# Kernel optimization log

Measured on AMD Instinct MI355X. Metric: run time of the kernel, lower is better.

## Reference

```python
import jax, jax.numpy as jnp
import numpy as np

OBS = 128; N_AGENT = 16; N_ACTION = 8; N_LAYER = 2; HID = 128
GE = 256; LE = 256; F1 = 512; F2 = 512


def _edges(batch_size, n):
    # all ordered pairs (i, j), i != j, within each sample; GCNConv adds self-loops
    i, j = np.meshgrid(np.arange(n), np.arange(n), indexing='ij')
    m = i != j
    src0, dst0 = i[m], j[m]                      # [n*(n-1)]
    off = (np.arange(batch_size) * n)[:, None]
    src = (src0[None, :] + off).reshape(-1)
    dst = (dst0[None, :] + off).reshape(-1)
    return jnp.asarray(src, jnp.int32), jnp.asarray(dst, jnp.int32)


def setup_inputs() -> dict:
    key = jax.random.key(0)
    ks = jax.random.split(key, 16)
    g = lambda k, shp, fan: jax.random.normal(k, shp, jnp.float32) / np.sqrt(fan)
    return {
        'obs_j': jax.random.normal(ks[0], (2048, N_AGENT, OBS), jnp.float32),
        'W_pre': g(ks[1], (OBS, HID), OBS), 'b_pre': jnp.zeros((HID,), jnp.float32),
        'W_gcn': g(ks[2], (N_LAYER, HID, HID), HID), 'b_gcn': jnp.zeros((N_LAYER, HID), jnp.float32),
        'W_post': g(ks[3], (HID, GE), HID), 'b_post': jnp.zeros((GE,), jnp.float32),
        'W_loc': g(ks[4], (OBS, LE), OBS), 'b_loc': jnp.zeros((LE,), jnp.float32),
        'W1': g(ks[5], (GE + LE, F1), GE + LE), 'b1': jnp.zeros((F1,), jnp.float32),
        'W2': g(ks[6], (F1, F2), F1), 'b2': jnp.zeros((F2,), jnp.float32),
        'W3': g(ks[7], (F2, N_ACTION), F2), 'b3': jnp.zeros((N_ACTION,), jnp.float32),
    }


def reference(obs_j, W_pre, b_pre, W_gcn, b_gcn, W_post, b_post,
              W_loc, b_loc, W1, b1, W2, b2, W3, b3):
    B, n, _ = obs_j.shape
    N = B * n
    obs = obs_j.reshape(N, OBS)
    x = jax.nn.relu(obs @ W_pre + b_pre)          # [N, HID]

    src, dst = _edges(B, n)
    # GCNConv with self-loops on a fully-connected graph: deg = n for every node,
    # edge norm = 1/sqrt(deg_i*deg_j) = 1/n for every (A+I) edge.
    inv_n = jnp.float32(1.0) / n
    for l in range(N_LAYER):
        h = x @ W_gcn[l]                          # lin (no bias inside propagate)
        agg = jax.ops.segment_sum(h[src], dst, num_segments=N)  # neighbor gather/scatter
        x = jax.nn.relu((agg + h) * inv_n + b_gcn[l])            # + self-loop msg, bias

    g = x.reshape(B, n, HID).mean(axis=1)         # global_mean_pool over each graph
    g = jax.nn.relu(g @ W_post + b_post)          # [B, GE]
    loc = jax.nn.relu(obs @ W_loc + b_loc)        # [B*n, LE]
    gi = jnp.repeat(g, n, axis=0)                 # repeat_interleave over agents
    z = jnp.concatenate([gi, loc], axis=1)
    z = jax.nn.relu(z @ W1 + b1)
    z = jax.nn.relu(z @ W2 + b2)
    q = z @ W3 + b3
    return q.reshape(B, n, N_ACTION)
```

## Files before the change

kernel.cpp:

```cpp
#include <hip/hip_runtime.h>
#include <hip/hip_bf16.h>
#include <stdint.h>

typedef __bf16 bf16;
typedef __bf16 bf16x4 __attribute__((ext_vector_type(4)));
typedef __bf16 bf16x8 __attribute__((ext_vector_type(8)));
typedef float f32x4 __attribute__((ext_vector_type(4)));

#define MFMA(a, b, c) __builtin_amdgcn_mfma_f32_16x16x32_bf16(a, b, c, 0, 0, 0)
#define GL(p) ((const __attribute__((address_space(1))) void*)(p))
#define SH(p) ((__attribute__((address_space(3))) void*)(p))

__device__ inline void tp(const float* W, bf16* WT, int id, int shiftK, int N) {
  int K = 1 << shiftK;
  int n = id >> shiftK;
  int k = id & (K - 1);
  WT[id] = (bf16)W[(size_t)k * N + n];
}

__global__ __launch_bounds__(256) void prep_all(
    const float* __restrict__ W1, const float* __restrict__ W2,
    bf16* __restrict__ W1T, bf16* __restrict__ W2T,
    const float* __restrict__ Wpre, const float* __restrict__ Wloc,
    const float* __restrict__ Wgcn, const float* __restrict__ Wpost,
    bf16* __restrict__ WpreLocT, bf16* __restrict__ Wg0T, bf16* __restrict__ Wg1T,
    bf16* __restrict__ WpostT,
    const float* __restrict__ bpre, const float* __restrict__ bloc,
    float* __restrict__ biasPL, float* __restrict__ outq) {
  __shared__ bf16 tile[64 * 68];
  int blk = blockIdx.x;
  int tid = threadIdx.x;
  if (blk < 128) {
    const float* W = (blk < 64) ? W1 : W2;
    bf16* WT = (blk < 64) ? W1T : W2T;
    int t = blk & 63;
    int tk0 = (t >> 3) * 64, tn0 = (t & 7) * 64;
#pragma unroll
    for (int p = 0; p < 4; p++) {
      int kr = p * 16 + (tid >> 4), nc = (tid & 15) * 4;
      float4 f = *(const float4*)(W + (size_t)(tk0 + kr) * 512 + tn0 + nc);
      bf16x4 v; v[0] = (bf16)f.x; v[1] = (bf16)f.y; v[2] = (bf16)f.z; v[3] = (bf16)f.w;
      *(bf16x4*)&tile[kr * 68 + nc] = v;
    }
    __syncthreads();
#pragma unroll
    for (int p = 0; p < 4; p++) {
      int nr = p * 16 + (tid >> 4), kc = (tid & 15) * 4;
      bf16x4 v;
#pragma unroll
      for (int i = 0; i < 4; i++) v[i] = tile[(kc + i) * 68 + nr];
      *(bf16x4*)(WT + (size_t)(tn0 + nr) * 512 + tk0 + kc) = v;
    }
    return;
  }
  blk -= 128;
  if (blk < 448) {
    int id = blk * 256 + tid;
    if (id < 16384) { tp(Wpre, WpreLocT, id, 7, 128); return; } id -= 16384;
    if (id < 32768) { tp(Wloc, WpreLocT + 16384, id, 7, 256); return; } id -= 32768;
    if (id < 16384) { tp(Wgcn, Wg0T, id, 7, 128); return; } id -= 16384;
    if (id < 16384) { tp(Wgcn + 16384, Wg1T, id, 7, 128); return; } id -= 16384;
    tp(Wpost, WpostT, id, 7, 256);
    return;
  }
  blk -= 448;
  if (blk == 0) {
    if (tid < 128) biasPL[tid] = bpre[tid];
    biasPL[128 + tid] = bloc[tid];
    return;
  }
  blk -= 1;
  float4 z = {0.f, 0.f, 0.f, 0.f};
#pragma unroll
  for (int i = 0; i < 4; i++)
    ((float4*)outq)[(size_t)blk * 1024 + i * 256 + tid] = z;
}

__global__ __launch_bounds__(256, 4) void k1c(
    const float* __restrict__ obs, const bf16* __restrict__ WpreLocT,
    const float* __restrict__ biasPL,
    const bf16* __restrict__ Wg0T, const bf16* __restrict__ Wg1T,
    const bf16* __restrict__ WpostT, const float* __restrict__ b_gcn,
    const float* __restrict__ b_post,
    const bf16* __restrict__ W1T, const float* __restrict__ b1,
    bf16* __restrict__ loc, float* __restrict__ h) {
  __shared__ bf16 smem[16384];

  const int tid = threadIdx.x;
  const int id = blockIdx.x;
  const int s = id >> 3;
  const int n_idx = s % 3;
  const int m0 = ((id & 7) + 8 * (s / 3)) * 128;
  const int n0 = n_idx * 128;

  f32x4 acc[4][4] = {};
  const int lane = tid & 63, wave = tid >> 6;
  const int wm = (wave >> 1) * 64, wn = (wave & 1) * 64;
  const int lm = lane & 15, quad = lane >> 4;

  float4 pa[4];

  auto loadA = [&](int kt) {
#pragma unroll
    for (int it = 0; it < 2; it++) {
      int idx = it * 256 + tid;
      int row = idx >> 2;
      int c = idx & 3;
      int cv = c ^ ((row >> 1) & 3);
      const float* src = obs + (size_t)(m0 + row) * 128 + kt * 32 + cv * 8;
      pa[it * 2] = *(const float4*)src;
      pa[it * 2 + 1] = *(const float4*)(src + 4);
    }
  };
  auto stageB = [&](int kt, int buf) {
    bf16* Bd = smem + buf * 8192 + 4096;
#pragma unroll
    for (int it = 0; it < 2; it++) {
      int idx = it * 256 + tid;
      int row = idx >> 2;
      int c = idx & 3;
      int cv = c ^ ((row >> 1) & 3);
      const bf16* gb = WpreLocT + (size_t)(n0 + row) * 128 + kt * 32 + cv * 8;
      __builtin_amdgcn_global_load_lds(GL(gb), SH(&Bd[(idx & ~63) * 8]), 16, 0, 0);
    }
  };
  auto commitA = [&](int buf) {
    bf16* Ad = smem + buf * 8192;
#pragma unroll
    for (int it = 0; it < 2; it++) {
      int idx = it * 256 + tid;
      int row = idx >> 2;
      int c = idx & 3;
      float4 f0 = pa[it * 2], f1 = pa[it * 2 + 1];
      bf16x8 v;
      v[0] = (bf16)f0.x; v[1] = (bf16)f0.y; v[2] = (bf16)f0.z; v[3] = (bf16)f0.w;
      v[4] = (bf16)f1.x; v[5] = (bf16)f1.y; v[6] = (bf16)f1.z; v[7] = (bf16)f1.w;
      *(bf16x8*)&Ad[row * 32 + c * 8] = v;
    }
  };
  auto compute = [&](int buf) {
    const bf16* Ar = smem + buf * 8192;
    const bf16* Br = smem + buf * 8192 + 4096;
    bf16x8 a[4], b[4];
#pragma unroll
    for (int i = 0; i < 4; i++) {
      int r = wm + lm + i * 16;
      a[i] = *(const bf16x8*)&Ar[r * 32 + ((quad ^ ((r >> 1) & 3)) * 8)];
    }
#pragma unroll
    for (int j = 0; j < 4; j++) {
      int r = wn + lm + j * 16;
      b[j] = *(const bf16x8*)&Br[r * 32 + ((quad ^ ((r >> 1) & 3)) * 8)];
    }
#pragma unroll
    for (int i = 0; i < 4; i++)
#pragma unroll
      for (int j = 0; j < 4; j++)
        acc[i][j] = MFMA(a[i], b[j], acc[i][j]);
  };

  loadA(0); stageB(0, 0); commitA(0);
  __syncthreads();
#pragma unroll
  for (int i = 0; i < 4; ++i) {
    if (i + 1 < 4) { loadA(i + 1); stageB(i + 1, (i + 1) & 1); }
    compute(i & 1);
    if (i + 1 < 4) commitA((i + 1) & 1);
    __syncthreads();
  }

  if (n_idx == 0) {
    bf16* xs = smem;
    bf16* x2 = smem + 2176;
    bf16* gS = smem + 4352;
#pragma unroll
    for (int i = 0; i < 4; i++) {
      int sl = (wave >> 1) * 4 + i;
#pragma unroll
      for (int j = 0; j < 4; j++) {
        int col = wn + j * 16 + lm;
        float bb = biasPL[col];
        float v = 0.f;
#pragma unroll
        for (int r = 0; r < 4; r++) v += fmaxf(acc[i][j][r] + bb, 0.f);
        v += __shfl_xor(v, 16);
        v += __shfl_xor(v, 32);
        if (quad == 0) xs[sl * 136 + col] = (bf16)(v * 0.0625f);
        else if (quad == 1) xs[(8 + sl) * 136 + col] = (bf16)0.f;
      }
    }
    __syncthreads();
    {
      f32x4 c2[2] = {};
#pragma unroll
      for (int ku = 0; ku < 4; ++ku) {
        bf16x8 a = *(const bf16x8*)&xs[lm * 136 + (ku * 4 + quad) * 8];
#pragma unroll
        for (int jn = 0; jn < 2; ++jn) {
          int col = (wave * 2 + jn) * 16 + lm;
          bf16x8 b = *(const bf16x8*)&Wg0T[(size_t)col * 128 + ku * 32 + quad * 8];
          c2[jn] = MFMA(a, b, c2[jn]);
        }
      }
      __syncthreads();
#pragma unroll
      for (int jn = 0; jn < 2; ++jn) {
        int col = (wave * 2 + jn) * 16 + lm;
        float bb = b_gcn[col];
#pragma unroll
        for (int r = 0; r < 4; ++r)
          x2[(quad * 4 + r) * 136 + col] = (bf16)fmaxf(c2[jn][r] + bb, 0.f);
      }
    }
    __syncthreads();
    {
      f32x4 c2[2] = {};
#pragma unroll
      for (int ku = 0; ku < 4; ++ku) {
        bf16x8 a = *(const bf16x8*)&x2[lm * 136 + (ku * 4 + quad) * 8];
#pragma unroll
        for (int jn = 0; jn < 2; ++jn) {
          int col = (wave * 2 + jn) * 16 + lm;
          bf16x8 b = *(const bf16x8*)&Wg1T[(size_t)col * 128 + ku * 32 + quad * 8];
          c2[jn] = MFMA(a, b, c2[jn]);
        }
      }
      __syncthreads();
#pragma unroll
      for (int jn = 0; jn < 2; ++jn) {
        int col = (wave * 2 + jn) * 16 + lm;
        float bb = b_gcn[128 + col];
#pragma unroll
        for (int r = 0; r < 4; ++r)
          xs[(quad * 4 + r) * 136 + col] = (bf16)fmaxf(c2[jn][r] + bb, 0.f);
      }
    }
    __syncthreads();
    {
      f32x4 c3[4] = {};
#pragma unroll
      for (int ku = 0; ku < 4; ++ku) {
        bf16x8 a = *(const bf16x8*)&xs[lm * 136 + (ku * 4 + quad) * 8];
#pragma unroll
        for (int jn = 0; jn < 4; ++jn) {
          int col = (wave * 4 + jn) * 16 + lm;
          bf16x8 b = *(const bf16x8*)&WpostT[(size_t)col * 128 + ku * 32 + quad * 8];
          c3[jn] = MFMA(a, b, c3[jn]);
        }
      }
#pragma unroll
      for (int jn = 0; jn < 4; ++jn) {
        int col = (wave * 4 + jn) * 16 + lm;
        float bb = b_post[col];
#pragma unroll
        for (int r = 0; r < 4; ++r)
          gS[(quad * 4 + r) * 264 + col] = (bf16)fmaxf(c3[jn][r] + bb, 0.f);
      }
    }
    __syncthreads();
    {
      f32x4 hacc[8] = {};
#pragma unroll
      for (int ku = 0; ku < 8; ++ku) {
        bf16x8 a = *(const bf16x8*)&gS[lm * 264 + ku * 32 + quad * 8];
#pragma unroll
        for (int jn = 0; jn < 8; ++jn) {
          int col = (wave * 8 + jn) * 16 + lm;
          bf16x8 b = *(const bf16x8*)&W1T[(size_t)col * 512 + ku * 32 + quad * 8];
          hacc[jn] = MFMA(a, b, hacc[jn]);
        }
      }
      int sample0 = m0 >> 4;
#pragma unroll
      for (int jn = 0; jn < 8; ++jn) {
        int col = (wave * 8 + jn) * 16 + lm;
        float bb = b1[col];
#pragma unroll
        for (int r = 0; r < 4; ++r) {
          int row = quad * 4 + r;
          if (row < 8)
            h[(size_t)(sample0 + row) * 512 + col] = hacc[jn][r] + bb;
        }
      }
    }
  } else {
#pragma unroll
    for (int i = 0; i < 4; i++)
#pragma unroll
      for (int j = 0; j < 4; j++) {
        int col = wn + j * 16 + lm;
        float bb = biasPL[n0 + col];
#pragma unroll
        for (int r = 0; r < 4; r++) {
          int row = wm + i * 16 + quad * 4 + r;
          smem[row * 128 + col] = (bf16)fmaxf(acc[i][j][r] + bb, 0.f);
        }
      }
    __syncthreads();
    const int coff = n0 - 128;
#pragma unroll
    for (int c = 0; c < 8; c++) {
      int ci = c * 256 + tid;
      int row = ci >> 4, col8 = (ci & 15) * 8;
      *(bf16x8*)&loc[(size_t)(m0 + row) * 256 + coff + col8] = *(const bf16x8*)&smem[row * 128 + col8];
    }
  }
}

template <bool HREP>
__global__ __launch_bounds__(256, 4) void gemm_k(
    const bf16* __restrict__ Ab, const bf16* __restrict__ BT,
    const float* __restrict__ bias, const float* __restrict__ hrep,
    bf16* __restrict__ C,
    const float* __restrict__ W3, const float* __restrict__ b3,
    float* __restrict__ outq) {
  __shared__ bf16 smem[16384];

  const int tid = threadIdx.x;
  const int id = blockIdx.x;
  const int s = id >> 3;
  const int n_idx = s & 3;
  const int m0 = ((id & 7) + 8 * (s >> 2)) * 128;
  const int n0 = n_idx * 128;

  f32x4 acc[4][4] = {};
  const int lane = tid & 63, wave = tid >> 6;
  const int wm = (wave >> 1) * 64, wn = (wave & 1) * 64;
  const int lm = lane & 15, quad = lane >> 4;

  auto stage = [&](int kt, int buf) {
    bf16* Ad = smem + buf * 8192;
    bf16* Bd = smem + buf * 8192 + 4096;
    int k0 = kt * 32;
#pragma unroll
    for (int it = 0; it < 2; it++) {
      int idx = it * 256 + tid;
      int row = idx >> 2;
      int c = idx & 3;
      int cv = c ^ ((row >> 1) & 3);
      int kk = k0 + cv * 8;
      const bf16* ga = HREP ? (Ab + (size_t)(m0 + row) * 256 + kk)
                            : (Ab + (size_t)(m0 + row) * 512 + kk);
      __builtin_amdgcn_global_load_lds(GL(ga), SH(&Ad[(idx & ~63) * 8]), 16, 0, 0);
      const bf16* gb = HREP ? (BT + (size_t)(n0 + row) * 512 + 256 + kk)
                            : (BT + (size_t)(n0 + row) * 512 + kk);
      __builtin_amdgcn_global_load_lds(GL(gb), SH(&Bd[(idx & ~63) * 8]), 16, 0, 0);
    }
  };

  auto compute = [&](int buf) {
    const bf16* Ar = smem + buf * 8192;
    const bf16* Br = smem + buf * 8192 + 4096;
    bf16x8 a[4], b[4];
#pragma unroll
    for (int i = 0; i < 4; i++) {
      int r = wm + lm + i * 16;
      a[i] = *(const bf16x8*)&Ar[r * 32 + ((quad ^ ((r >> 1) & 3)) * 8)];
    }
#pragma unroll
    for (int j = 0; j < 4; j++) {
      int r = wn + lm + j * 16;
      b[j] = *(const bf16x8*)&Br[r * 32 + ((quad ^ ((r >> 1) & 3)) * 8)];
    }
#pragma unroll
    for (int i = 0; i < 4; i++)
#pragma unroll
      for (int j = 0; j < 4; j++)
        acc[i][j] = MFMA(a[i], b[j], acc[i][j]);
  };

  const int NIT = HREP ? 8 : 16;
  stage(0, 0);
  __syncthreads();
#pragma unroll 2
  for (int i = 0; i < NIT; ++i) {
    if (i + 1 < NIT) stage(i + 1, (i + 1) & 1);
    compute(i & 1);
    __syncthreads();
  }

  if (HREP) {
#pragma unroll
    for (int i = 0; i < 4; i++) {
      int sample = (m0 + wm + i * 16) >> 4;
#pragma unroll
      for (int j = 0; j < 4; j++) {
        int col = n0 + wn + j * 16 + lm;
        float hv = hrep[(size_t)sample * 512 + col];
#pragma unroll
        for (int r = 0; r < 4; r++) {
          int row = wm + i * 16 + quad * 4 + r;
          smem[row * 128 + (col - n0)] = (bf16)fmaxf(acc[i][j][r] + hv, 0.f);
        }
      }
    }
    __syncthreads();
#pragma unroll
    for (int c = 0; c < 8; c++) {
      int ci = c * 256 + tid;
      int row = ci >> 4, col8 = (ci & 15) * 8;
      *(bf16x8*)&C[(size_t)(m0 + row) * 512 + n0 + col8] = *(const bf16x8*)&smem[row * 128 + col8];
    }
  } else {
#pragma unroll
    for (int i = 0; i < 4; i++)
#pragma unroll
      for (int j = 0; j < 4; j++) {
        int col = wn + j * 16 + lm;
        float bb = bias[n0 + col];
#pragma unroll
        for (int r = 0; r < 4; r++) {
          int row = wm + i * 16 + quad * 4 + r;
          smem[row * 128 + col] = (bf16)fmaxf(acc[i][j][r] + bb, 0.f);
        }
      }
    __syncthreads();
    int n = lane & 7;
    int kg = lane >> 3;
    float w3r[16];
#pragma unroll
    for (int i = 0; i < 16; i++) w3r[i] = W3[(size_t)(n0 + kg * 16 + i) * 8 + n];
    float bn = (n_idx == 0) ? b3[n] : 0.f;
    int rbase = wave * 32;
    for (int rr = 0; rr < 32; rr++) {
      const bf16* zr = &smem[(rbase + rr) * 128 + kg * 16];
      bf16x8 z0 = *(const bf16x8*)zr;
      bf16x8 z1v = *(const bf16x8*)(zr + 8);
      float v = 0.f;
#pragma unroll
      for (int i = 0; i < 8; i++) v += (float)z0[i] * w3r[i];
#pragma unroll
      for (int i = 0; i < 8; i++) v += (float)z1v[i] * w3r[8 + i];
      v += __shfl_down(v, 32);
      v += __shfl_down(v, 16);
      v += __shfl_down(v, 8);
      if (lane < 8) atomicAdd(&outq[(size_t)(m0 + rbase + rr) * 8 + n], v + bn);
    }
  }
}

extern "C" void kernel_launch(void* const* d_in, const int* in_sizes, int n_in,
                              void* d_out, int out_size, void* d_ws, size_t ws_size,
                              hipStream_t stream) {
  const float* obs    = (const float*)d_in[0];
  const float* W_pre  = (const float*)d_in[1];
  const float* b_pre  = (const float*)d_in[2];
  const float* W_gcn  = (const float*)d_in[3];
  const float* b_gcn  = (const float*)d_in[4];
  const float* W_post = (const float*)d_in[5];
  const float* b_post = (const float*)d_in[6];
  const float* W_loc  = (const float*)d_in[7];
  const float* b_loc  = (const float*)d_in[8];
  const float* W1     = (const float*)d_in[9];
  const float* b1     = (const float*)d_in[10];
  const float* W2     = (const float*)d_in[11];
  const float* b2     = (const float*)d_in[12];
  const float* W3     = (const float*)d_in[13];
  const float* b3     = (const float*)d_in[14];
  float* out = (float*)d_out;

  char* p = (char*)d_ws;
  auto alloc = [&](size_t bytes) { char* r = p; p += (bytes + 255) & ~(size_t)255; return r; };
  bf16* WpreLocT = (bf16*)alloc(384 * 128 * 2);
  float* biasPL  = (float*)alloc(384 * 4);
  bf16* Wg0T   = (bf16*)alloc(128 * 128 * 2);
  bf16* Wg1T   = (bf16*)alloc(128 * 128 * 2);
  bf16* WpostT = (bf16*)alloc(256 * 128 * 2);
  bf16* W1T    = (bf16*)alloc(512 * 512 * 2);
  bf16* W2T    = (bf16*)alloc(512 * 512 * 2);
  bf16* locB   = (bf16*)alloc((size_t)32768 * 256 * 2);
  float* hB    = (float*)alloc((size_t)2048 * 512 * 4);
  bf16* z1B    = (bf16*)alloc((size_t)32768 * 512 * 2);

  prep_all<<<641, 256, 0, stream>>>(W1, W2, W1T, W2T,
                                    W_pre, W_loc, W_gcn, W_post,
                                    WpreLocT, Wg0T, Wg1T, WpostT,
                                    b_pre, b_loc, biasPL, out);
  k1c<<<768, 256, 0, stream>>>(obs, WpreLocT, biasPL,
                               Wg0T, Wg1T, WpostT, b_gcn, b_post,
                               W1T, b1, locB, hB);
  gemm_k<true><<<1024, 256, 0, stream>>>(locB, W1T, nullptr, hB, z1B,
                                         nullptr, nullptr, nullptr);
  gemm_k<false><<<1024, 256, 0, stream>>>(z1B, W2T, b2, nullptr, nullptr,
                                          W3, b3, out);
}
```

Before: 162.6 us.

## Fuse the W1, W2 and W3 GEMMs into one kernel with z1 kept in LDS

The two gemm_k launches are replaced by a single kernel in which each block owns 128 rows. The block computes the full 512-wide z1 into a swizzled 128 KB LDS buffer, then runs the W2 GEMM against it and applies W3 via MFMA using a hi/lo bf16 split of W3. This removes the global round trip of z1, the output zeroing, and the per-row atomics. The cost is one block per CU with only 256 blocks, large LDS use and less latency hiding, and the intra-block W1T and W2T streaming is now serialized over four column chunks.

```diff
diff --git a/kernel.cpp b/kernel.cpp
--- a/kernel.cpp
+++ b/kernel.cpp
@@ -26,7 +26,8 @@
     bf16* __restrict__ WpreLocT, bf16* __restrict__ Wg0T, bf16* __restrict__ Wg1T,
     bf16* __restrict__ WpostT,
     const float* __restrict__ bpre, const float* __restrict__ bloc,
-    float* __restrict__ biasPL, float* __restrict__ outq) {
+    float* __restrict__ biasPL,
+    const float* __restrict__ W3, bf16* __restrict__ W3bT) {
   __shared__ bf16 tile[64 * 68];
   int blk = blockIdx.x;
   int tid = threadIdx.x;
@@ -69,11 +70,15 @@
     biasPL[128 + tid] = bloc[tid];
     return;
   }
-  blk -= 1;
-  float4 z = {0.f, 0.f, 0.f, 0.f};
-#pragma unroll
-  for (int i = 0; i < 4; i++)
-    ((float4*)outq)[(size_t)blk * 1024 + i * 256 + tid] = z;
+#pragma unroll
+  for (int i = 0; i < 32; i++) {
+    int id = i * 256 + tid;
+    int n = id >> 9, k = id & 511;
+    float w = (n < 8) ? W3[(size_t)k * 8 + n] : 0.f;
+    bf16 hi = (bf16)w;
+    W3bT[id] = hi;
+    W3bT[8192 + id] = (bf16)(w - (float)hi);
+  }
 }
 
 __global__ __launch_bounds__(256, 4) void k1c(
@@ -307,136 +312,173 @@
   }
 }
 
-template <bool HREP>
-__global__ __launch_bounds__(256, 4) void gemm_k(
-    const bf16* __restrict__ Ab, const bf16* __restrict__ BT,
-    const float* __restrict__ bias, const float* __restrict__ hrep,
-    bf16* __restrict__ C,
-    const float* __restrict__ W3, const float* __restrict__ b3,
-    float* __restrict__ outq) {
-  __shared__ bf16 smem[16384];
+__global__ __launch_bounds__(256, 1) void k34(
+    const bf16* __restrict__ locB, const bf16* __restrict__ W1T,
+    const float* __restrict__ hB, const bf16* __restrict__ W2T,
+    const float* __restrict__ b2, const bf16* __restrict__ W3bT,
+    const float* __restrict__ b3, float* __restrict__ outq) {
+  __shared__ bf16 smem[81920];
+  bf16* const z1 = smem;
+  bf16* const stg = smem + 65536;
 
   const int tid = threadIdx.x;
-  const int id = blockIdx.x;
-  const int s = id >> 3;
-  const int n_idx = s & 3;
-  const int m0 = ((id & 7) + 8 * (s >> 2)) * 128;
-  const int n0 = n_idx * 128;
-
-  f32x4 acc[4][4] = {};
+  const int m0 = blockIdx.x * 128;
   const int lane = tid & 63, wave = tid >> 6;
   const int wm = (wave >> 1) * 64, wn = (wave & 1) * 64;
   const int lm = lane & 15, quad = lane >> 4;
 
-  auto stage = [&](int kt, int buf) {
-    bf16* Ad = smem + buf * 8192;
-    bf16* Bd = smem + buf * 8192 + 4096;
-    int k0 = kt * 32;
-#pragma unroll
-    for (int it = 0; it < 2; it++) {
-      int idx = it * 256 + tid;
-      int row = idx >> 2;
-      int c = idx & 3;
-      int cv = c ^ ((row >> 1) & 3);
-      int kk = k0 + cv * 8;
-      const bf16* ga = HREP ? (Ab + (size_t)(m0 + row) * 256 + kk)
-                            : (Ab + (size_t)(m0 + row) * 512 + kk);
-      __builtin_amdgcn_global_load_lds(GL(ga), SH(&Ad[(idx & ~63) * 8]), 16, 0, 0);
-      const bf16* gb = HREP ? (BT + (size_t)(n0 + row) * 512 + 256 + kk)
-                            : (BT + (size_t)(n0 + row) * 512 + kk);
-      __builtin_amdgcn_global_load_lds(GL(gb), SH(&Bd[(idx & ~63) * 8]), 16, 0, 0);
-    }
-  };
-
-  auto compute = [&](int buf) {
-    const bf16* Ar = smem + buf * 8192;
-    const bf16* Br = smem + buf * 8192 + 4096;
-    bf16x8 a[4], b[4];
-#pragma unroll
-    for (int i = 0; i < 4; i++) {
-      int r = wm + lm + i * 16;
-      a[i] = *(const bf16x8*)&Ar[r * 32 + ((quad ^ ((r >> 1) & 3)) * 8)];
-    }
-#pragma unroll
-    for (int j = 0; j < 4; j++) {
-      int r = wn + lm + j * 16;
-      b[j] = *(const bf16x8*)&Br[r * 32 + ((quad ^ ((r >> 1) & 3)) * 8)];
-    }
-#pragma unroll
-    for (int i = 0; i < 4; i++)
-#pragma unroll
-      for (int j = 0; j < 4; j++)
-        acc[i][j] = MFMA(a[i], b[j], acc[i][j]);
-  };
-
-  const int NIT = HREP ? 8 : 16;
-  stage(0, 0);
-  __syncthreads();
+  f32x4 qacc[2] = {};
+
+  for (int nc = 0; nc < 4; ++nc) {
+    f32x4 acc[4][4] = {};
+    auto stage1 = [&](int kt, int buf) {
+      bf16* Ad = stg + buf * 8192;
+      bf16* Bd = stg + buf * 8192 + 4096;
+#pragma unroll
+      for (int it = 0; it < 2; it++) {
+        int idx = it * 256 + tid;
+        int row = idx >> 2;
+        int c = idx & 3;
+        int cv = c ^ ((row >> 1) & 3);
+        int kk = kt * 32 + cv * 8;
+        const bf16* ga = locB + (size_t)(m0 + row) * 256 + kk;
+        __builtin_amdgcn_global_load_lds(GL(ga), SH(&Ad[(idx & ~63) * 8]), 16, 0, 0);
+        const bf16* gb = W1T + (size_t)(nc * 128 + row) * 512 + 256 + kk;
+        __builtin_amdgcn_global_load_lds(GL(gb), SH(&Bd[(idx & ~63) * 8]), 16, 0, 0);
+      }
+    };
+    auto compute1 = [&](int buf) {
+      const bf16* Ar = stg + buf * 8192;
+      const bf16* Br = stg + buf * 8192 + 4096;
+      bf16x8 a[4], b[4];
+#pragma unroll
+      for (int i = 0; i < 4; i++) {
+        int r = wm + lm + i * 16;
+        a[i] = *(const bf16x8*)&Ar[r * 32 + ((quad ^ ((r >> 1) & 3)) * 8)];
+      }
+#pragma unroll
+      for (int j = 0; j < 4; j++) {
+        int r = wn + lm + j * 16;
+        b[j] = *(const bf16x8*)&Br[r * 32 + ((quad ^ ((r >> 1) & 3)) * 8)];
+      }
+#pragma unroll
+      for (int i = 0; i < 4; i++)
+#pragma unroll
+        for (int j = 0; j < 4; j++)
+          acc[i][j] = MFMA(a[i], b[j], acc[i][j]);
+    };
+
+    stage1(0, 0);
+    __syncthreads();
 #pragma unroll 2
-  for (int i = 0; i < NIT; ++i) {
-    if (i + 1 < NIT) stage(i + 1, (i + 1) & 1);
-    compute(i & 1);
-    __syncthreads();
-  }
-
-  if (HREP) {
+    for (int kt = 0; kt < 8; ++kt) {
+      if (kt + 1 < 8) stage1(kt + 1, (kt + 1) & 1);
+      compute1(kt & 1);
+      __syncthreads();
+    }
 #pragma unroll
     for (int i = 0; i < 4; i++) {
       int sample = (m0 + wm + i * 16) >> 4;
 #pragma unroll
       for (int j = 0; j < 4; j++) {
-        int col = n0 + wn + j * 16 + lm;
-        float hv = hrep[(size_t)sample * 512 + col];
+        int col = nc * 128 + wn + j * 16 + lm;
+        float hv = hB[(size_t)sample * 512 + col];
 #pragma unroll
         for (int r = 0; r < 4; r++) {
           int row = wm + i * 16 + quad * 4 + r;
-          smem[row * 128 + (col - n0)] = (bf16)fmaxf(acc[i][j][r] + hv, 0.f);
-        }
-      }
-    }
-    __syncthreads();
-#pragma unroll
-    for (int c = 0; c < 8; c++) {
-      int ci = c * 256 + tid;
-      int row = ci >> 4, col8 = (ci & 15) * 8;
-      *(bf16x8*)&C[(size_t)(m0 + row) * 512 + n0 + col8] = *(const bf16x8*)&smem[row * 128 + col8];
-    }
-  } else {
-#pragma unroll
-    for (int i = 0; i < 4; i++)
+          int pc = (col >> 3) ^ (row & 7);
+          z1[row * 512 + pc * 8 + (col & 7)] = (bf16)fmaxf(acc[i][j][r] + hv, 0.f);
+        }
+      }
+    }
+  }
+  __syncthreads();
+
+  for (int nc = 0; nc < 4; ++nc) {
+    f32x4 acc[4][4] = {};
+    auto stage2 = [&](int kt, int buf) {
+      bf16* Bd = stg + buf * 8192 + 4096;
+#pragma unroll
+      for (int it = 0; it < 2; it++) {
+        int idx = it * 256 + tid;
+        int row = idx >> 2;
+        int c = idx & 3;
+        int cv = c ^ ((row >> 1) & 3);
+        const bf16* gb = W2T + (size_t)(nc * 128 + row) * 512 + kt * 32 + cv * 8;
+        __builtin_amdgcn_global_load_lds(GL(gb), SH(&Bd[(idx & ~63) * 8]), 16, 0, 0);
+      }
+    };
+    auto compute2 = [&](int kt, int buf) {
+      const bf16* Br = stg + buf * 8192 + 4096;
+      bf16x8 a[4], b[4];
+#pragma unroll
+      for (int i = 0; i < 4; i++) {
+        int r = wm + lm + i * 16;
+        a[i] = *(const bf16x8*)&z1[r * 512 + (((kt * 4 + quad) ^ (r & 7)) * 8)];
+      }
 #pragma unroll
       for (int j = 0; j < 4; j++) {
-        int col = wn + j * 16 + lm;
-        float bb = bias[n0 + col];
+        int r = wn + lm + j * 16;
+        b[j] = *(const bf16x8*)&Br[r * 32 + ((quad ^ ((r >> 1) & 3)) * 8)];
+      }
+#pragma unroll
+      for (int i = 0; i < 4; i++)
+#pragma unroll
+        for (int j = 0; j < 4; j++)
+          acc[i][j] = MFMA(a[i], b[j], acc[i][j]);
+    };
+
+    stage2(0, 0);
+    __syncthreads();
+#pragma unroll 2
+    for (int kt = 0; kt < 16; ++kt) {
+      if (kt + 1 < 16) stage2(kt + 1, (kt + 1) & 1);
+      compute2(kt, kt & 1);
+      __syncthreads();
+    }
+#pragma unroll
+    for (int j = 0; j < 4; j++) {
+      float bb = b2[nc * 128 + wn + j * 16 + lm];
+#pragma unroll
+      for (int i = 0; i < 4; i++) {
 #pragma unroll
         for (int r = 0; r < 4; r++) {
           int row = wm + i * 16 + quad * 4 + r;
-          smem[row * 128 + col] = (bf16)fmaxf(acc[i][j][r] + bb, 0.f);
-        }
-      }
-    __syncthreads();
-    int n = lane & 7;
-    int kg = lane >> 3;
-    float w3r[16];
-#pragma unroll
-    for (int i = 0; i < 16; i++) w3r[i] = W3[(size_t)(n0 + kg * 16 + i) * 8 + n];
-    float bn = (n_idx == 0) ? b3[n] : 0.f;
-    int rbase = wave * 32;
-    for (int rr = 0; rr < 32; rr++) {
-      const bf16* zr = &smem[(rbase + rr) * 128 + kg * 16];
-      bf16x8 z0 = *(const bf16x8*)zr;
-      bf16x8 z1v = *(const bf16x8*)(zr + 8);
-      float v = 0.f;
-#pragma unroll
-      for (int i = 0; i < 8; i++) v += (float)z0[i] * w3r[i];
-#pragma unroll
-      for (int i = 0; i < 8; i++) v += (float)z1v[i] * w3r[8 + i];
-      v += __shfl_down(v, 32);
-      v += __shfl_down(v, 16);
-      v += __shfl_down(v, 8);
-      if (lane < 8) atomicAdd(&outq[(size_t)(m0 + rbase + rr) * 8 + n], v + bn);
-    }
-  }
+          int col = wn + j * 16 + lm;
+          int pc = (col >> 3) ^ (row & 7);
+          stg[row * 128 + pc * 8 + (col & 7)] = (bf16)fmaxf(acc[i][j][r] + bb, 0.f);
+        }
+      }
+    }
+    __syncthreads();
+    {
+      bf16x8 w3h[4], w3l[4];
+#pragma unroll
+      for (int kt = 0; kt < 4; kt++) {
+        w3h[kt] = *(const bf16x8*)&W3bT[lm * 512 + nc * 128 + kt * 32 + quad * 8];
+        w3l[kt] = *(const bf16x8*)&W3bT[8192 + lm * 512 + nc * 128 + kt * 32 + quad * 8];
+      }
+#pragma unroll
+      for (int it = 0; it < 2; it++) {
+#pragma unroll
+        for (int kt = 0; kt < 4; kt++) {
+          int r = wave * 32 + it * 16 + lm;
+          bf16x8 a = *(const bf16x8*)&stg[r * 128 + (((kt * 4 + quad) ^ (r & 7)) * 8)];
+          qacc[it] = MFMA(a, w3h[kt], qacc[it]);
+          qacc[it] = MFMA(a, w3l[kt], qacc[it]);
+        }
+      }
+    }
+    __syncthreads();
+  }
+
+#pragma unroll
+  for (int it = 0; it < 2; it++)
+#pragma unroll
+    for (int r = 0; r < 4; r++) {
+      int row = m0 + wave * 32 + it * 16 + quad * 4 + r;
+      if (lm < 8) outq[(size_t)row * 8 + lm] = qacc[it][r] + b3[lm];
+    }
 }
 
 extern "C" void kernel_launch(void* const* d_in, const int* in_sizes, int n_in,
@@ -468,19 +510,16 @@
   bf16* WpostT = (bf16*)alloc(256 * 128 * 2);
   bf16* W1T    = (bf16*)alloc(512 * 512 * 2);
   bf16* W2T    = (bf16*)alloc(512 * 512 * 2);
+  bf16* W3bT   = (bf16*)alloc(2 * 16 * 512 * 2);
   bf16* locB   = (bf16*)alloc((size_t)32768 * 256 * 2);
   float* hB    = (float*)alloc((size_t)2048 * 512 * 4);
-  bf16* z1B    = (bf16*)alloc((size_t)32768 * 512 * 2);
-
-  prep_all<<<641, 256, 0, stream>>>(W1, W2, W1T, W2T,
+
+  prep_all<<<578, 256, 0, stream>>>(W1, W2, W1T, W2T,
                                     W_pre, W_loc, W_gcn, W_post,
                                     WpreLocT, Wg0T, Wg1T, WpostT,
-                                    b_pre, b_loc, biasPL, out);
+                                    b_pre, b_loc, biasPL, W3, W3bT);
   k1c<<<768, 256, 0, stream>>>(obs, WpreLocT, biasPL,
                                Wg0T, Wg1T, WpostT, b_gcn, b_post,
                                W1T, b1, locB, hB);
-  gemm_k<true><<<1024, 256, 0, stream>>>(locB, W1T, nullptr, hB, z1B,
-                                         nullptr, nullptr, nullptr);
-  gemm_k<false><<<1024, 256, 0, stream>>>(z1B, W2T, b2, nullptr, nullptr,
-                                          W3, b3, out);
+  k34<<<256, 256, 0, stream>>>(locB, W1T, hB, W2T, b2, W3bT, b3, out);
 }
```

Result: slower. 180.1 us (+10.8%).
